# Kernel optimization log

Hardware: AMD Instinct MI355X
Metric: run time of the kernel (lower is better)

Reference implementation:

```python
import jax, jax.numpy as jnp
import numpy as np

NUM_HEADS = 4
LN_EPS = 1e-5


def setup_inputs() -> dict:
    key = jax.random.key(0)
    B, S, D = 4, 2048, 1024
    H = NUM_HEADS
    hd = D // H
    ks = jax.random.split(key, 8)
    s = 1.0 / np.sqrt(hd)
    inp = {
        "embeddings": jax.random.normal(ks[0], (B, S, D), dtype=jnp.float32),
        # per-head Q/K/V projection weights (torch Linear weight layout [out,in])
        "Wq": jax.random.normal(ks[1], (H, hd, hd), dtype=jnp.float32) * s,
        "Wk": jax.random.normal(ks[2], (H, hd, hd), dtype=jnp.float32) * s,
        "Wv": jax.random.normal(ks[3], (H, hd, hd), dtype=jnp.float32) * s,
        # lens bias scalars: causal, intent, temporal, normative (init values from module)
        "bias_scalars": jnp.array([0.1, 0.15, 0.05, 0.2], dtype=jnp.float32),
        "Wo_w": jax.random.normal(ks[4], (D, D), dtype=jnp.float32) / np.sqrt(D),
        "Wo_b": jnp.zeros((D,), dtype=jnp.float32),
        "ln_g": jnp.ones((D,), dtype=jnp.float32),
        "ln_b": jnp.zeros((D,), dtype=jnp.float32),
    }
    return inp


def _legal_biases(x, bias_scalars):
    """x: [B,H,S,hd] per-head embeddings. Returns stacked bias [B,H,S,S]."""
    B, H, S, hd = x.shape
    # head 0: CAUSAL -> strictly upper triangular mask * causal_bias
    causal = jnp.triu(jnp.ones((S, S), dtype=x.dtype), k=1)  # [S,S]
    b0 = causal[None] * bias_scalars[0]                      # [1,S,S] -> bcast B
    b0 = jnp.broadcast_to(b0, (B, S, S))
    # head 1: INTENTIONALITY -> outer product of embedding norms, global-mean threshold
    mag1 = jnp.linalg.norm(x[:, 1], axis=-1)                 # [B,S]
    intent = mag1[:, :, None] * mag1[:, None, :]             # [B,S,S]
    b1 = (intent > intent.mean()).astype(x.dtype) * bias_scalars[1]
    # head 2: TEMPORAL -> exp(-|i-j|/S)
    pos = jnp.arange(S, dtype=x.dtype)
    prox = jnp.exp(-jnp.abs(pos[:, None] - pos[None, :]) / S)  # [S,S]
    b2 = jnp.broadcast_to(prox[None] * bias_scalars[2], (B, S, S))
    # head 3: NORMATIVE -> outer product of last feature, > 0.5 threshold
    v3 = x[:, 3, :, -1]                                      # [B,S]
    viol = v3[:, :, None] * v3[:, None, :]                   # [B,S,S]
    b3 = (viol > 0.5).astype(x.dtype) * bias_scalars[3]
    return jnp.stack([b0, b1, b2, b3], axis=1)               # [B,H,S,S]


def _forward(embeddings, Wq, Wk, Wv, bias_scalars, Wo_w, Wo_b, ln_g, ln_b):
    B, S, D = embeddings.shape
    H = NUM_HEADS
    hd = D // H
    x = embeddings.reshape(B, S, H, hd).transpose(0, 2, 1, 3)     # [B,H,S,hd]
    # torch Linear: y = x @ W.T
    Q = jnp.einsum('bhsd,hed->bhse', x, Wq)
    K = jnp.einsum('bhsd,hed->bhse', x, Wk)
    V = jnp.einsum('bhsd,hed->bhse', x, Wv)
    scores = jnp.einsum('bhse,bhte->bhst', Q, K) / np.sqrt(hd)    # [B,H,S,S]
    scores = scores + _legal_biases(x, bias_scalars)
    weights = jax.nn.softmax(scores, axis=-1)                     # [B,H,S,S]
    attended = jnp.einsum('bhst,bhte->bhse', weights, V)          # [B,H,S,hd]
    concat = attended.transpose(0, 2, 1, 3).reshape(B, S, D)      # head order = concat order
    out = concat @ Wo_w.T + Wo_b
    # layer_norm(out + embeddings)
    y = out + embeddings
    mu = y.mean(axis=-1, keepdims=True)
    var = ((y - mu) ** 2).mean(axis=-1, keepdims=True)
    output = (y - mu) / jnp.sqrt(var + LN_EPS) * ln_g + ln_b      # [B,S,D]
    average_weights = weights.mean(axis=1)                        # [B,S,S]
    guilt = jax.nn.softmax(average_weights.sum(axis=-1), axis=-1) # [B,S]
    return output, average_weights, guilt


def reference(embeddings, Wq, Wk, Wv, bias_scalars, Wo_w, Wo_b, ln_g, ln_b):
    return _forward(embeddings, Wq, Wk, Wv, bias_scalars, Wo_w, Wo_b, ln_g, ln_b)
```

## Files before the change

kernel.cpp:

```cpp
#include <hip/hip_runtime.h>
#include <hip/hip_bf16.h>
#include <math.h>

#define S_ 2048
#define D_ 1024
#define H_ 4
#define HD_ 256
#define B_ 4

typedef __hip_bfloat16 bf16;
typedef short s16x8 __attribute__((ext_vector_type(8)));
typedef float f32x4 __attribute__((ext_vector_type(4)));

#define GLOAD16(g, l)                                             \
    __builtin_amdgcn_global_load_lds(                             \
        (const __attribute__((address_space(1))) void*)(g),       \
        (__attribute__((address_space(3))) void*)(l), 16, 0, 0)

template <int MODE>
__global__ __launch_bounds__(256) void mfma_nt(
    int K,
    const bf16* __restrict__ A, int lda, long sA_b, long sA_h,
    const bf16* __restrict__ Bm, int ldb, long sB_b, long sB_h,
    void* __restrict__ Cp, int ldc, long sC_b, long sC_h,
    int zdiv, int bbase,
    const double* __restrict__ mag1d, const double* __restrict__ v3d,
    const double* __restrict__ meand, const float* __restrict__ bias_sc)
{
    __shared__ __align__(16) short As[128 * 32];
    __shared__ __align__(16) short Bs[128 * 32];

    const int tid = threadIdx.x;
    const int w = tid >> 6, lane = tid & 63;
    const int srow = lane >> 2, scol = (lane & 3) << 3;
    const int quad = lane >> 4, r = lane & 15;
    const int wr = (w >> 1) * 64, wc = (w & 1) * 64;
    const int zb = blockIdx.z / zdiv, zh = blockIdx.z % zdiv;

    const bf16* Ap = A + (size_t)zb * sA_b + (size_t)zh * sA_h +
                     (size_t)blockIdx.y * 128 * lda;
    const bf16* Bp = Bm + (size_t)zb * sB_b + (size_t)zh * sB_h +
                     (size_t)blockIdx.x * 128 * ldb;

    f32x4 acc[4][4] = {};

    for (int k0 = 0; k0 < K; k0 += 32) {
        if (k0) __syncthreads();
#pragma unroll
        for (int l = 0; l < 2; l++) {
            GLOAD16(Ap + (size_t)(w * 32 + l * 16 + srow) * lda + (k0 + scol),
                    &As[(w * 32 + l * 16) * 32]);
            GLOAD16(Bp + (size_t)(w * 32 + l * 16 + srow) * ldb + (k0 + scol),
                    &Bs[(w * 32 + l * 16) * 32]);
        }
        __syncthreads();

        s16x8 af[4], bfv[4];
        const s16x8* A8 = (const s16x8*)As;
        const s16x8* B8 = (const s16x8*)Bs;
#pragma unroll
        for (int i = 0; i < 4; i++) af[i] = A8[(wr + i * 16 + r) * 4 + quad];
#pragma unroll
        for (int j = 0; j < 4; j++) bfv[j] = B8[(wc + j * 16 + r) * 4 + quad];
#pragma unroll
        for (int i = 0; i < 4; i++)
#pragma unroll
            for (int j = 0; j < 4; j++)
                acc[i][j] = __builtin_amdgcn_mfma_f32_16x16x32_bf16(
                    af[i], bfv[j], acc[i][j], 0, 0, 0);
    }

    const int row0 = blockIdx.y * 128 + wr + quad * 4;
    const int col0 = blockIdx.x * 128 + wc + r;

    if (MODE == 0) {
        float* C = (float*)Cp + (size_t)zb * sC_b + (size_t)zh * sC_h;
#pragma unroll
        for (int i = 0; i < 4; i++)
#pragma unroll
            for (int j = 0; j < 4; j++)
#pragma unroll
                for (int p = 0; p < 4; p++)
                    C[(size_t)(row0 + i * 16 + p) * ldc + (col0 + j * 16)] = acc[i][j][p];
    } else if (MODE == 1) {
        bf16* C = (bf16*)Cp + (size_t)zb * sC_b + (size_t)zh * sC_h;
#pragma unroll
        for (int i = 0; i < 4; i++)
#pragma unroll
            for (int j = 0; j < 4; j++)
#pragma unroll
                for (int p = 0; p < 4; p++)
                    C[(size_t)(row0 + i * 16 + p) * ldc + (col0 + j * 16)] =
                        __float2bfloat16(acc[i][j][p]);
    } else {
        float* C = (float*)Cp + (size_t)zb * sC_b + (size_t)zh * sC_h;
        const int h = zh;
        const int bbatch = bbase + zb;
        const float bsc = bias_sc[h];
        if (h == 0) {
#pragma unroll
            for (int i = 0; i < 4; i++)
#pragma unroll
                for (int j = 0; j < 4; j++)
#pragma unroll
                    for (int p = 0; p < 4; p++) {
                        const int rr = row0 + i * 16 + p, c = col0 + j * 16;
                        C[(size_t)rr * ldc + c] = acc[i][j][p] + ((c > rr) ? bsc : 0.0f);
                    }
        } else if (h == 2) {
#pragma unroll
            for (int i = 0; i < 4; i++)
#pragma unroll
                for (int j = 0; j < 4; j++)
#pragma unroll
                    for (int p = 0; p < 4; p++) {
                        const int rr = row0 + i * 16 + p, c = col0 + j * 16;
                        int d = c - rr; d = d < 0 ? -d : d;
                        C[(size_t)rr * ldc + c] =
                            acc[i][j][p] + bsc * expf(-(float)d * (1.0f / 2048.0f));
                    }
        } else {
            const double* src = (h == 1) ? mag1d : v3d;
            const double thr = (h == 1) ? meand[0] : 0.5;
            double rv[16], cv[4];
#pragma unroll
            for (int i = 0; i < 4; i++)
#pragma unroll
                for (int p = 0; p < 4; p++)
                    rv[i * 4 + p] = src[(size_t)bbatch * S_ + row0 + i * 16 + p];
#pragma unroll
            for (int j = 0; j < 4; j++)
                cv[j] = src[(size_t)bbatch * S_ + col0 + j * 16];
#pragma unroll
            for (int i = 0; i < 4; i++)
#pragma unroll
                for (int j = 0; j < 4; j++)
#pragma unroll
                    for (int p = 0; p < 4; p++) {
                        const int rr = row0 + i * 16 + p, c = col0 + j * 16;
                        C[(size_t)rr * ldc + c] =
                            acc[i][j][p] + ((rv[i * 4 + p] * cv[j] > thr) ? bsc : 0.0f);
                    }
        }
    }
}

__global__ __launch_bounds__(256) void cvt_bf16(const float* __restrict__ in,
                                                bf16* __restrict__ out, int n,
                                                float scale) {
    const size_t i0 = ((size_t)blockIdx.x * 256 + threadIdx.x) * 4;
    if (i0 + 3 < (size_t)n) {
        const float4 v = *(const float4*)(in + i0);
        out[i0 + 0] = __float2bfloat16(v.x * scale);
        out[i0 + 1] = __float2bfloat16(v.y * scale);
        out[i0 + 2] = __float2bfloat16(v.z * scale);
        out[i0 + 3] = __float2bfloat16(v.w * scale);
    }
}

__global__ __launch_bounds__(256) void transpose_v(const bf16* __restrict__ in,
                                                   bf16* __restrict__ out) {
    const int h = blockIdx.z / B_, b = blockIdx.z % B_;
    const int e0 = blockIdx.x * 64, s0 = blockIdx.y * 64;
    __shared__ short t[64][66];
    const int tid = threadIdx.x;
    const int rr = tid >> 2;
    const int cc = (tid & 3) << 4;
    const bf16* ip = in + (((size_t)h * B_ * S_) + (size_t)b * S_ + s0) * HD_ + e0;
    const s16x8 v0 = *(const s16x8*)(ip + (size_t)rr * HD_ + cc);
    const s16x8 v1 = *(const s16x8*)(ip + (size_t)rr * HD_ + cc + 8);
#pragma unroll
    for (int i = 0; i < 8; i++) {
        t[rr][cc + i] = v0[i];
        t[rr][cc + 8 + i] = v1[i];
    }
    __syncthreads();
    bf16* op = out + (((size_t)h * B_ + b) * HD_ + e0 + rr) * S_ + s0 + cc;
    s16x8 o0, o1;
#pragma unroll
    for (int i = 0; i < 8; i++) {
        o0[i] = t[cc + i][rr];
        o1[i] = t[cc + 8 + i][rr];
    }
    *(s16x8*)op = o0;
    *(s16x8*)(op + 8) = o1;
}

__global__ __launch_bounds__(256) void prep_kernel(const float* __restrict__ emb,
                                                   double* __restrict__ mag1d,
                                                   double* __restrict__ v3d) {
    const long row = blockIdx.x;
    const int tid = threadIdx.x;
    const float x = emb[row * D_ + 256 + tid];
    __shared__ double red[256];
    red[tid] = (double)x * (double)x;
    __syncthreads();
    for (int off = 128; off > 0; off >>= 1) {
        if (tid < off) red[tid] += red[tid + off];
        __syncthreads();
    }
    if (tid == 0) {
        mag1d[row] = sqrt(red[0]);
        v3d[row] = (double)emb[row * D_ + 1023];
    }
}

__global__ __launch_bounds__(256) void mean_kernel(const double* __restrict__ mag1d,
                                                   double* __restrict__ meand) {
    const int tid = threadIdx.x;
    __shared__ double red[256];
    double acc = 0.0;
    for (int b = 0; b < B_; b++) {
        double ss = 0.0;
        for (int i = tid; i < S_; i += 256) ss += mag1d[(long)b * S_ + i];
        __syncthreads();
        red[tid] = ss;
        __syncthreads();
        for (int off = 128; off > 0; off >>= 1) {
            if (tid < off) red[tid] += red[tid + off];
            __syncthreads();
        }
        if (tid == 0) {
            const double rb = red[0] / (double)S_;
            acc += rb * rb;
        }
        __syncthreads();
    }
    if (tid == 0) meand[0] = acc / (double)B_;
}

__global__ __launch_bounds__(256) void softmax_fused(
    const float* __restrict__ scores, bf16* __restrict__ P, long p_h, int p_row,
    float* __restrict__ avgw, float* __restrict__ rowsum) {
    const int s = blockIdx.x, tid = threadIdx.x;
    __shared__ float red[256];
    float wacc[8] = {0, 0, 0, 0, 0, 0, 0, 0};
    for (int h = 0; h < H_; h++) {
        const float* rp = scores + ((size_t)h * S_ + s) * S_;
        bf16* pp = P + (size_t)h * p_h + (size_t)s * p_row;
        float v[8];
        float m = -1e30f;
#pragma unroll
        for (int i = 0; i < 8; i++) {
            v[i] = rp[tid + 256 * i];
            m = fmaxf(m, v[i]);
        }
        red[tid] = m;
        __syncthreads();
        for (int off = 128; off > 0; off >>= 1) {
            if (tid < off) red[tid] = fmaxf(red[tid], red[tid + off]);
            __syncthreads();
        }
        m = red[0];
        __syncthreads();
        float sum = 0.0f;
#pragma unroll
        for (int i = 0; i < 8; i++) {
            v[i] = expf(v[i] - m);
            sum += v[i];
        }
        red[tid] = sum;
        __syncthreads();
        for (int off = 128; off > 0; off >>= 1) {
            if (tid < off) red[tid] += red[tid + off];
            __syncthreads();
        }
        const float inv = 1.0f / red[0];
        __syncthreads();
#pragma unroll
        for (int i = 0; i < 8; i++) {
            const float wv = v[i] * inv;
            pp[tid + 256 * i] = __float2bfloat16(wv);
            wacc[i] += wv;
        }
    }
    float asum = 0.0f;
#pragma unroll
    for (int i = 0; i < 8; i++) {
        const float a = wacc[i] * 0.25f;
        avgw[(size_t)s * S_ + tid + 256 * i] = a;
        asum += a;
    }
    red[tid] = asum;
    __syncthreads();
    for (int off = 128; off > 0; off >>= 1) {
        if (tid < off) red[tid] += red[tid + off];
        __syncthreads();
    }
    if (tid == 0) rowsum[s] = red[0];
}

__global__ __launch_bounds__(256) void ln_kernel(float* __restrict__ out,
                                                 const float* __restrict__ emb,
                                                 const float* __restrict__ wob,
                                                 const float* __restrict__ g,
                                                 const float* __restrict__ beta) {
    const long row = blockIdx.x;
    float* o = out + row * D_;
    const float* e = emb + row * D_;
    const int tid = threadIdx.x;
    __shared__ float red[256];
    float v[4];
    float sum = 0.0f;
#pragma unroll
    for (int i = 0; i < 4; i++) {
        const int c = tid + 256 * i;
        v[i] = o[c] + wob[c] + e[c];
        sum += v[i];
    }
    red[tid] = sum;
    __syncthreads();
    for (int off = 128; off > 0; off >>= 1) {
        if (tid < off) red[tid] += red[tid + off];
        __syncthreads();
    }
    const float mu = red[0] * (1.0f / 1024.0f);
    __syncthreads();
    float vs = 0.0f;
#pragma unroll
    for (int i = 0; i < 4; i++) {
        const float d = v[i] - mu;
        vs += d * d;
    }
    red[tid] = vs;
    __syncthreads();
    for (int off = 128; off > 0; off >>= 1) {
        if (tid < off) red[tid] += red[tid + off];
        __syncthreads();
    }
    const float var = red[0] * (1.0f / 1024.0f);
    const float inv = 1.0f / sqrtf(var + 1e-5f);
#pragma unroll
    for (int i = 0; i < 4; i++) {
        const int c = tid + 256 * i;
        o[c] = (v[i] - mu) * inv * g[c] + beta[c];
    }
}

__global__ __launch_bounds__(256) void guilt_kernel(const float* __restrict__ rowsum,
                                                    float* __restrict__ guilt) {
    const int b = blockIdx.x, tid = threadIdx.x;
    const float* r = rowsum + (long)b * S_;
    float* gq = guilt + (long)b * S_;
    __shared__ float red[256];
    float v[8];
    float m = -1e30f;
#pragma unroll
    for (int i = 0; i < 8; i++) {
        v[i] = r[tid + 256 * i];
        m = fmaxf(m, v[i]);
    }
    red[tid] = m;
    __syncthreads();
    for (int off = 128; off > 0; off >>= 1) {
        if (tid < off) red[tid] = fmaxf(red[tid], red[tid + off]);
        __syncthreads();
    }
    m = red[0];
    __syncthreads();
    float sum = 0.0f;
#pragma unroll
    for (int i = 0; i < 8; i++) {
        v[i] = expf(v[i] - m);
        sum += v[i];
    }
    red[tid] = sum;
    __syncthreads();
    for (int off = 128; off > 0; off >>= 1) {
        if (tid < off) red[tid] += red[tid + off];
        __syncthreads();
    }
    const float inv = 1.0f / red[0];
#pragma unroll
    for (int i = 0; i < 8; i++) gq[tid + 256 * i] = v[i] * inv;
}

extern "C" void kernel_launch(void* const* d_in, const int* in_sizes, int n_in,
                              void* d_out, int out_size, void* d_ws, size_t ws_size,
                              hipStream_t stream) {
    const float* emb = (const float*)d_in[0];
    const float* Wq = (const float*)d_in[1];
    const float* Wk = (const float*)d_in[2];
    const float* Wv = (const float*)d_in[3];
    const float* bias_sc = (const float*)d_in[4];
    const float* Wo_w = (const float*)d_in[5];
    const float* Wo_b = (const float*)d_in[6];
    const float* ln_g = (const float*)d_in[7];
    const float* ln_bt = (const float*)d_in[8];

    char* ws = (char*)d_ws;
    size_t off = 0;
    auto alloc = [&](size_t bytes) {
        size_t o = off;
        off = (off + bytes + 255) & ~(size_t)255;
        return o;
    };
    bf16* embb = (bf16*)(ws + alloc((size_t)B_ * S_ * D_ * 2));
    bf16* concat = embb;
    bf16* Qm = (bf16*)(ws + alloc((size_t)H_ * B_ * S_ * HD_ * 2));
    bf16* Km = (bf16*)(ws + alloc((size_t)H_ * B_ * S_ * HD_ * 2));
    bf16* Vtb = (bf16*)(ws + alloc((size_t)H_ * B_ * HD_ * S_ * 2));
    bf16* Wqb = (bf16*)(ws + alloc((size_t)H_ * HD_ * HD_ * 2));
    bf16* Wkb = (bf16*)(ws + alloc((size_t)H_ * HD_ * HD_ * 2));
    bf16* Wvb = (bf16*)(ws + alloc((size_t)H_ * HD_ * HD_ * 2));
    bf16* Wob = (bf16*)(ws + alloc((size_t)D_ * D_ * 2));
    double* mag1d = (double*)(ws + alloc((size_t)B_ * S_ * 8));
    double* v3d = (double*)(ws + alloc((size_t)B_ * S_ * 8));
    double* meand = (double*)(ws + alloc(256));
    float* rowsum = (float*)(ws + alloc((size_t)B_ * S_ * 4));
    float* scores = (float*)(ws + alloc((size_t)H_ * S_ * S_ * 4));
    bf16* Vraw = (bf16*)scores;
    bf16* P = (bf16*)(ws + off);
    const size_t need_batched = off + (size_t)B_ * H_ * S_ * S_ * 2;
    const bool batched = ws_size >= need_batched;

    float* outp = (float*)d_out;
    float* avgw = outp + (size_t)B_ * S_ * D_;
    float* guilt = avgw + (size_t)B_ * S_ * S_;

    cvt_bf16<<<(B_ * S_ * D_) / 1024, 256, 0, stream>>>(emb, embb, B_ * S_ * D_, 1.0f);
    cvt_bf16<<<(H_ * HD_ * HD_) / 1024, 256, 0, stream>>>(Wq, Wqb, H_ * HD_ * HD_, 0.0625f);
    cvt_bf16<<<(H_ * HD_ * HD_) / 1024, 256, 0, stream>>>(Wk, Wkb, H_ * HD_ * HD_, 1.0f);
    cvt_bf16<<<(H_ * HD_ * HD_) / 1024, 256, 0, stream>>>(Wv, Wvb, H_ * HD_ * HD_, 1.0f);
    cvt_bf16<<<(D_ * D_) / 1024, 256, 0, stream>>>(Wo_w, Wob, D_ * D_, 1.0f);

    prep_kernel<<<B_ * S_, 256, 0, stream>>>(emb, mag1d, v3d);
    mean_kernel<<<1, 256, 0, stream>>>(mag1d, meand);

    {
        const dim3 g(HD_ / 128, (B_ * S_) / 128, H_);
        const long sQ = (long)B_ * S_ * HD_;
        mfma_nt<1><<<g, 256, 0, stream>>>(HD_, embb, D_, 0, HD_,
                                          Wqb, HD_, 0, (long)HD_ * HD_,
                                          Qm, HD_, 0, sQ, H_, 0,
                                          nullptr, nullptr, nullptr, nullptr);
        mfma_nt<1><<<g, 256, 0, stream>>>(HD_, embb, D_, 0, HD_,
                                          Wkb, HD_, 0, (long)HD_ * HD_,
                                          Km, HD_, 0, sQ, H_, 0,
                                          nullptr, nullptr, nullptr, nullptr);
        mfma_nt<1><<<g, 256, 0, stream>>>(HD_, embb, D_, 0, HD_,
                                          Wvb, HD_, 0, (long)HD_ * HD_,
                                          Vraw, HD_, 0, sQ, H_, 0,
                                          nullptr, nullptr, nullptr, nullptr);
    }
    transpose_v<<<dim3(HD_ / 64, S_ / 64, H_ * B_), 256, 0, stream>>>(Vraw, Vtb);

    for (int b = 0; b < B_; b++) {
        mfma_nt<3><<<dim3(S_ / 128, S_ / 128, H_), 256, 0, stream>>>(
            HD_,
            Qm + (size_t)b * S_ * HD_, HD_, 0, (long)B_ * S_ * HD_,
            Km + (size_t)b * S_ * HD_, HD_, 0, (long)B_ * S_ * HD_,
            scores, S_, 0, (long)S_ * S_,
            H_, b, mag1d, v3d, meand, bias_sc);
        if (batched) {
            softmax_fused<<<S_, 256, 0, stream>>>(
                scores, P + (size_t)b * H_ * S_ * S_, (long)S_ * S_, S_,
                avgw + (size_t)b * S_ * S_, rowsum + (size_t)b * S_);
        } else {
            softmax_fused<<<S_, 256, 0, stream>>>(
                scores, (bf16*)scores, 2L * S_ * S_, 2 * S_,
                avgw + (size_t)b * S_ * S_, rowsum + (size_t)b * S_);
            mfma_nt<1><<<dim3(HD_ / 128, S_ / 128, H_), 256, 0, stream>>>(
                S_,
                (const bf16*)scores, 2 * S_, 0, 2L * S_ * S_,
                Vtb + (size_t)b * HD_ * S_, S_, 0, (long)B_ * HD_ * S_,
                concat + (size_t)b * S_ * D_, D_, 0, HD_,
                H_, 0, nullptr, nullptr, nullptr, nullptr);
        }
    }
    if (batched) {
        mfma_nt<1><<<dim3(HD_ / 128, S_ / 128, B_ * H_), 256, 0, stream>>>(
            S_,
            P, S_, (long)H_ * S_ * S_, (long)S_ * S_,
            Vtb, S_, (long)HD_ * S_, (long)B_ * HD_ * S_,
            concat, D_, (long)S_ * D_, HD_,
            H_, 0, nullptr, nullptr, nullptr, nullptr);
    }

    mfma_nt<0><<<dim3(D_ / 128, (B_ * S_) / 128, 1), 256, 0, stream>>>(
        D_, concat, D_, 0, 0, Wob, D_, 0, 0, outp, D_, 0, 0,
        1, 0, nullptr, nullptr, nullptr, nullptr);

    ln_kernel<<<B_ * S_, 256, 0, stream>>>(outp, emb, Wo_b, ln_g, ln_bt);
    guilt_kernel<<<B_, 256, 0, stream>>>(rowsum, guilt);
}
```

Before: 524.4 us.

## Add dedicated 128x256-tile PV matmul kernel with swizzled block mapping

Replaces the generic P·V matmul launch with a specialized 512-thread kernel. Each block computes a 128x256 output tile covering a full head dimension, so each P row-block is read once instead of twice. It double-buffers K-slices in LDS using direct global-to-LDS loads. The block index is remapped so that concurrently running blocks share batch-head slices. This trades higher LDS and register use per block for less P traffic and fewer launches.

```diff
diff --git a/kernel.cpp b/kernel.cpp
--- a/kernel.cpp
+++ b/kernel.cpp
@@ -143,6 +143,76 @@
                     }
         }
     }
+}
+
+__global__ __launch_bounds__(512) void mfma_pv(const bf16* __restrict__ Pm,
+                                               const bf16* __restrict__ Vt,
+                                               bf16* __restrict__ Cc) {
+    __shared__ __align__(16) short L[2][12288];
+
+    const int tid = threadIdx.x;
+    const int w = tid >> 6, lane = tid & 63;
+    const int quad = lane >> 4, r = lane & 15;
+    const int wr = (w >> 2) * 64, wc = (w & 3) * 64;
+
+    const int bid = blockIdx.x;
+    const int bh = (bid & 7) * 2 + ((bid >> 3) >> 4);
+    const int rb = (bid >> 3) & 15;
+    const int b = bh >> 2, h = bh & 3;
+
+    const bf16* Ap = Pm + ((size_t)bh * S_ + (size_t)rb * 128) * S_;
+    const bf16* Bp = Vt + (size_t)(h * B_ + b) * HD_ * S_;
+
+    const int srow = tid >> 2, scol = (tid & 3) << 3;
+    const int wbase = w * 512;
+
+    f32x4 acc[4][4] = {};
+
+    auto stage = [&](int bs, int k0) {
+        short* sb = &L[bs][0];
+        GLOAD16(Ap + (size_t)srow * S_ + (k0 + scol), sb + wbase);
+        GLOAD16(Bp + (size_t)srow * S_ + (k0 + scol), sb + 4096 + wbase);
+        GLOAD16(Bp + (size_t)(128 + srow) * S_ + (k0 + scol), sb + 8192 + wbase);
+    };
+    auto compute = [&](int bs) {
+        const s16x8* A8 = (const s16x8*)&L[bs][0];
+        const s16x8* B8 = (const s16x8*)&L[bs][4096];
+        s16x8 af[4], bfv[4];
+#pragma unroll
+        for (int i = 0; i < 4; i++) af[i] = A8[(wr + i * 16 + r) * 4 + quad];
+#pragma unroll
+        for (int j = 0; j < 4; j++) bfv[j] = B8[(wc + j * 16 + r) * 4 + quad];
+#pragma unroll
+        for (int i = 0; i < 4; i++)
+#pragma unroll
+            for (int j = 0; j < 4; j++)
+                acc[i][j] = __builtin_amdgcn_mfma_f32_16x16x32_bf16(
+                    af[i], bfv[j], acc[i][j], 0, 0, 0);
+    };
+
+    stage(0, 0);
+    __syncthreads();
+    int cur = 0;
+#pragma unroll 1
+    for (int t = 0; t < 63; ++t) {
+        stage(cur ^ 1, (t + 1) * 32);
+        compute(cur);
+        __syncthreads();
+        cur ^= 1;
+    }
+    compute(cur);
+
+    const int row0 = rb * 128 + wr + quad * 4;
+    const int col0 = h * HD_ + wc + r;
+    bf16* C = Cc + (size_t)b * S_ * D_;
+#pragma unroll
+    for (int i = 0; i < 4; i++)
+#pragma unroll
+        for (int j = 0; j < 4; j++)
+#pragma unroll
+            for (int p = 0; p < 4; p++)
+                C[(size_t)(row0 + i * 16 + p) * D_ + col0 + j * 16] =
+                    __float2bfloat16(acc[i][j][p]);
 }
 
 __global__ __launch_bounds__(256) void cvt_bf16(const float* __restrict__ in,
@@ -469,12 +539,7 @@
         }
     }
     if (batched) {
-        mfma_nt<1><<<dim3(HD_ / 128, S_ / 128, B_ * H_), 256, 0, stream>>>(
-            S_,
-            P, S_, (long)H_ * S_ * S_, (long)S_ * S_,
-            Vtb, S_, (long)HD_ * S_, (long)B_ * HD_ * S_,
-            concat, D_, (long)S_ * D_, HD_,
-            H_, 0, nullptr, nullptr, nullptr, nullptr);
+        mfma_pv<<<256, 512, 0, stream>>>(P, Vtb, concat);
     }
 
     mfma_nt<0><<<dim3(D_ / 128, (B_ * S_) / 128, 1), 256, 0, stream>>>(
```

New measurement: 521.4 us. Within noise of the previous version (-0.6%).

## Fuse softmax with PV matmul, swizzle GEMM LDS, vectorize layernorm

Applied to the files above, without the earlier changes.

Replaces the separate softmax kernel plus batched PV GEMM with a single kernel that computes per-row softmax stats, then streams normalized probabilities through LDS into MFMA against V, also producing averaged weights and row sums. This avoids writing and rereading the bf16 probability tensor. The GEMM's LDS layout gets an XOR swizzle to reduce bank conflicts, and layernorm uses float4 accesses. The fused kernel launches only S/16 blocks per batch and rereads V from global/L2 per block, which may limit occupancy and bandwidth.

```diff
diff --git a/kernel.cpp b/kernel.cpp
--- a/kernel.cpp
+++ b/kernel.cpp
@@ -16,6 +16,13 @@
     __builtin_amdgcn_global_load_lds(                             \
         (const __attribute__((address_space(1))) void*)(g),       \
         (__attribute__((address_space(3))) void*)(l), 16, 0, 0)
+
+static __device__ inline short bfb(float x) {
+    bf16 t = __float2bfloat16(x);
+    short s;
+    __builtin_memcpy(&s, &t, 2);
+    return s;
+}
 
 template <int MODE>
 __global__ __launch_bounds__(256) void mfma_nt(
@@ -32,8 +39,10 @@
 
     const int tid = threadIdx.x;
     const int w = tid >> 6, lane = tid & 63;
-    const int srow = lane >> 2, scol = (lane & 3) << 3;
+    const int srow = lane >> 2;
+    const int scol = (((lane & 3) ^ (srow & 3)) << 3);
     const int quad = lane >> 4, r = lane & 15;
+    const int qx = quad ^ (r & 3);
     const int wr = (w >> 1) * 64, wc = (w & 1) * 64;
     const int zb = blockIdx.z / zdiv, zh = blockIdx.z % zdiv;
 
@@ -59,9 +68,9 @@
         const s16x8* A8 = (const s16x8*)As;
         const s16x8* B8 = (const s16x8*)Bs;
 #pragma unroll
-        for (int i = 0; i < 4; i++) af[i] = A8[(wr + i * 16 + r) * 4 + quad];
-#pragma unroll
-        for (int j = 0; j < 4; j++) bfv[j] = B8[(wc + j * 16 + r) * 4 + quad];
+        for (int i = 0; i < 4; i++) af[i] = A8[(wr + i * 16 + r) * 4 + qx];
+#pragma unroll
+        for (int j = 0; j < 4; j++) bfv[j] = B8[(wc + j * 16 + r) * 4 + qx];
 #pragma unroll
         for (int i = 0; i < 4; i++)
 #pragma unroll
@@ -143,6 +152,119 @@
                     }
         }
     }
+}
+
+__global__ __launch_bounds__(512) void fused_smpv(
+    const float* __restrict__ scores,
+    const bf16* __restrict__ Vt,
+    int b,
+    bf16* __restrict__ Cc,
+    float* __restrict__ avgw_b,
+    float* __restrict__ rowsum_b)
+{
+    __shared__ __align__(16) short Pb[2][4][16 * 32];
+
+    const int tid = threadIdx.x;
+    const int rr = tid >> 5;
+    const int c32 = tid & 31;
+    const int r0 = blockIdx.x * 16;
+
+    const int w = tid >> 6, lane = tid & 63;
+    const int quad = lane >> 4, r = lane & 15;
+    const int n0 = w * 32;
+
+    const bf16* vh[4];
+#pragma unroll
+    for (int h = 0; h < 4; h++)
+        vh[h] = Vt + ((size_t)h * B_ + b) * HD_ * S_;
+
+    const float* sp[4];
+#pragma unroll
+    for (int h = 0; h < 4; h++)
+        sp[h] = scores + ((size_t)h * S_ + r0 + rr) * S_;
+
+    float mh[4], inv[4];
+#pragma unroll
+    for (int h = 0; h < 4; h++) {
+        const float4* rp4 = (const float4*)sp[h];
+        float4 v[16];
+#pragma unroll
+        for (int j = 0; j < 16; j++) v[j] = rp4[c32 + j * 32];
+        float m = -1e30f;
+#pragma unroll
+        for (int j = 0; j < 16; j++) {
+            m = fmaxf(m, fmaxf(fmaxf(v[j].x, v[j].y), fmaxf(v[j].z, v[j].w)));
+        }
+#pragma unroll
+        for (int d = 16; d; d >>= 1) m = fmaxf(m, __shfl_xor(m, d, 32));
+        float s = 0.f;
+#pragma unroll
+        for (int j = 0; j < 16; j++) {
+            s += expf(v[j].x - m);
+            s += expf(v[j].y - m);
+            s += expf(v[j].z - m);
+            s += expf(v[j].w - m);
+        }
+#pragma unroll
+        for (int d = 16; d; d >>= 1) s += __shfl_xor(s, d, 32);
+        mh[h] = m;
+        inv[h] = 1.0f / s;
+    }
+
+    f32x4 acc[4][2] = {};
+    float rs = 0.f;
+    float sv[4], svn[4];
+#pragma unroll
+    for (int h = 0; h < 4; h++) sv[h] = sp[h][c32];
+
+#pragma unroll 1
+    for (int t = 0; t < 64; ++t) {
+        const int k0 = t * 32;
+        const int buf = t & 1;
+        float wacc = 0.f;
+#pragma unroll
+        for (int h = 0; h < 4; h++) {
+            const float wv = expf(sv[h] - mh[h]) * inv[h];
+            wacc += wv;
+            Pb[buf][h][rr * 32 + c32] = bfb(wv);
+        }
+        const float aw = wacc * 0.25f;
+        avgw_b[(size_t)(r0 + rr) * S_ + k0 + c32] = aw;
+        rs += aw;
+        const int kn = (t < 63) ? k0 + 32 : k0;
+#pragma unroll
+        for (int h = 0; h < 4; h++) svn[h] = sp[h][kn + c32];
+
+        asm volatile("s_waitcnt lgkmcnt(0)" ::: "memory");
+        __builtin_amdgcn_s_barrier();
+        __builtin_amdgcn_sched_barrier(0);
+
+#pragma unroll
+        for (int h = 0; h < 4; h++) {
+            const s16x8 af = *(const s16x8*)&Pb[buf][h][r * 32 + quad * 8];
+            const s16x8 b0 =
+                *(const s16x8*)(vh[h] + (size_t)(n0 + r) * S_ + k0 + quad * 8);
+            const s16x8 b1 =
+                *(const s16x8*)(vh[h] + (size_t)(n0 + 16 + r) * S_ + k0 + quad * 8);
+            acc[h][0] = __builtin_amdgcn_mfma_f32_16x16x32_bf16(af, b0, acc[h][0], 0, 0, 0);
+            acc[h][1] = __builtin_amdgcn_mfma_f32_16x16x32_bf16(af, b1, acc[h][1], 0, 0, 0);
+        }
+#pragma unroll
+        for (int h = 0; h < 4; h++) sv[h] = svn[h];
+    }
+
+#pragma unroll
+    for (int d = 16; d; d >>= 1) rs += __shfl_xor(rs, d, 32);
+    if (c32 == 0) rowsum_b[r0 + rr] = rs;
+
+#pragma unroll
+    for (int h = 0; h < 4; h++)
+#pragma unroll
+        for (int j = 0; j < 2; j++)
+#pragma unroll
+            for (int p = 0; p < 4; p++)
+                Cc[(size_t)(r0 + quad * 4 + p) * D_ + h * HD_ + n0 + j * 16 + r] =
+                    __float2bfloat16(acc[h][j][p]);
 }
 
 __global__ __launch_bounds__(256) void cvt_bf16(const float* __restrict__ in,
@@ -229,67 +351,6 @@
     if (tid == 0) meand[0] = acc / (double)B_;
 }
 
-__global__ __launch_bounds__(256) void softmax_fused(
-    const float* __restrict__ scores, bf16* __restrict__ P, long p_h, int p_row,
-    float* __restrict__ avgw, float* __restrict__ rowsum) {
-    const int s = blockIdx.x, tid = threadIdx.x;
-    __shared__ float red[256];
-    float wacc[8] = {0, 0, 0, 0, 0, 0, 0, 0};
-    for (int h = 0; h < H_; h++) {
-        const float* rp = scores + ((size_t)h * S_ + s) * S_;
-        bf16* pp = P + (size_t)h * p_h + (size_t)s * p_row;
-        float v[8];
-        float m = -1e30f;
-#pragma unroll
-        for (int i = 0; i < 8; i++) {
-            v[i] = rp[tid + 256 * i];
-            m = fmaxf(m, v[i]);
-        }
-        red[tid] = m;
-        __syncthreads();
-        for (int off = 128; off > 0; off >>= 1) {
-            if (tid < off) red[tid] = fmaxf(red[tid], red[tid + off]);
-            __syncthreads();
-        }
-        m = red[0];
-        __syncthreads();
-        float sum = 0.0f;
-#pragma unroll
-        for (int i = 0; i < 8; i++) {
-            v[i] = expf(v[i] - m);
-            sum += v[i];
-        }
-        red[tid] = sum;
-        __syncthreads();
-        for (int off = 128; off > 0; off >>= 1) {
-            if (tid < off) red[tid] += red[tid + off];
-            __syncthreads();
-        }
-        const float inv = 1.0f / red[0];
-        __syncthreads();
-#pragma unroll
-        for (int i = 0; i < 8; i++) {
-            const float wv = v[i] * inv;
-            pp[tid + 256 * i] = __float2bfloat16(wv);
-            wacc[i] += wv;
-        }
-    }
-    float asum = 0.0f;
-#pragma unroll
-    for (int i = 0; i < 8; i++) {
-        const float a = wacc[i] * 0.25f;
-        avgw[(size_t)s * S_ + tid + 256 * i] = a;
-        asum += a;
-    }
-    red[tid] = asum;
-    __syncthreads();
-    for (int off = 128; off > 0; off >>= 1) {
-        if (tid < off) red[tid] += red[tid + off];
-        __syncthreads();
-    }
-    if (tid == 0) rowsum[s] = red[0];
-}
-
 __global__ __launch_bounds__(256) void ln_kernel(float* __restrict__ out,
                                                  const float* __restrict__ emb,
                                                  const float* __restrict__ wob,
@@ -300,15 +361,12 @@
     const float* e = emb + row * D_;
     const int tid = threadIdx.x;
     __shared__ float red[256];
-    float v[4];
-    float sum = 0.0f;
-#pragma unroll
-    for (int i = 0; i < 4; i++) {
-        const int c = tid + 256 * i;
-        v[i] = o[c] + wob[c] + e[c];
-        sum += v[i];
-    }
-    red[tid] = sum;
+    const float4 vo = ((const float4*)o)[tid];
+    const float4 vw = ((const float4*)wob)[tid];
+    const float4 ve = ((const float4*)e)[tid];
+    float v[4] = {vo.x + vw.x + ve.x, vo.y + vw.y + ve.y,
+                  vo.z + vw.z + ve.z, vo.w + vw.w + ve.w};
+    red[tid] = v[0] + v[1] + v[2] + v[3];
     __syncthreads();
     for (int off = 128; off > 0; off >>= 1) {
         if (tid < off) red[tid] += red[tid + off];
@@ -330,11 +388,14 @@
     }
     const float var = red[0] * (1.0f / 1024.0f);
     const float inv = 1.0f / sqrtf(var + 1e-5f);
-#pragma unroll
-    for (int i = 0; i < 4; i++) {
-        const int c = tid + 256 * i;
-        o[c] = (v[i] - mu) * inv * g[c] + beta[c];
-    }
+    const float4 g4 = ((const float4*)g)[tid];
+    const float4 b4 = ((const float4*)beta)[tid];
+    float4 r4;
+    r4.x = (v[0] - mu) * inv * g4.x + b4.x;
+    r4.y = (v[1] - mu) * inv * g4.y + b4.y;
+    r4.z = (v[2] - mu) * inv * g4.z + b4.z;
+    r4.w = (v[3] - mu) * inv * g4.w + b4.w;
+    ((float4*)o)[tid] = r4;
 }
 
 __global__ __launch_bounds__(256) void guilt_kernel(const float* __restrict__ rowsum,
@@ -410,9 +471,6 @@
     float* rowsum = (float*)(ws + alloc((size_t)B_ * S_ * 4));
     float* scores = (float*)(ws + alloc((size_t)H_ * S_ * S_ * 4));
     bf16* Vraw = (bf16*)scores;
-    bf16* P = (bf16*)(ws + off);
-    const size_t need_batched = off + (size_t)B_ * H_ * S_ * S_ * 2;
-    const bool batched = ws_size >= need_batched;
 
     float* outp = (float*)d_out;
     float* avgw = outp + (size_t)B_ * S_ * D_;
@@ -452,29 +510,11 @@
             Km + (size_t)b * S_ * HD_, HD_, 0, (long)B_ * S_ * HD_,
             scores, S_, 0, (long)S_ * S_,
             H_, b, mag1d, v3d, meand, bias_sc);
-        if (batched) {
-            softmax_fused<<<S_, 256, 0, stream>>>(
-                scores, P + (size_t)b * H_ * S_ * S_, (long)S_ * S_, S_,
-                avgw + (size_t)b * S_ * S_, rowsum + (size_t)b * S_);
-        } else {
-            softmax_fused<<<S_, 256, 0, stream>>>(
-                scores, (bf16*)scores, 2L * S_ * S_, 2 * S_,
-                avgw + (size_t)b * S_ * S_, rowsum + (size_t)b * S_);
-            mfma_nt<1><<<dim3(HD_ / 128, S_ / 128, H_), 256, 0, stream>>>(
-                S_,
-                (const bf16*)scores, 2 * S_, 0, 2L * S_ * S_,
-                Vtb + (size_t)b * HD_ * S_, S_, 0, (long)B_ * HD_ * S_,
-                concat + (size_t)b * S_ * D_, D_, 0, HD_,
-                H_, 0, nullptr, nullptr, nullptr, nullptr);
-        }
-    }
-    if (batched) {
-        mfma_nt<1><<<dim3(HD_ / 128, S_ / 128, B_ * H_), 256, 0, stream>>>(
-            S_,
-            P, S_, (long)H_ * S_ * S_, (long)S_ * S_,
-            Vtb, S_, (long)HD_ * S_, (long)B_ * HD_ * S_,
-            concat, D_, (long)S_ * D_, HD_,
-            H_, 0, nullptr, nullptr, nullptr, nullptr);
+        fused_smpv<<<S_ / 16, 512, 0, stream>>>(
+            scores, Vtb, b,
+            concat + (size_t)b * S_ * D_,
+            avgw + (size_t)b * S_ * S_,
+            rowsum + (size_t)b * S_);
     }
 
     mfma_nt<0><<<dim3(D_ / 128, (B_ * S_) / 128, 1), 256, 0, stream>>>(
```

After: 978.3 us. 1.87x slower.
